# Kernel optimization log

Hardware: AMD Instinct MI355X
Metric: run time of the kernel (lower is better)

## Reference

```python
import jax, jax.numpy as jnp
import numpy as np

N_NODES = 50000
NODE_DIM = 128
HIDDEN = 128
N_EDGES = 1600000
N_POSTS = 8192


def setup_inputs() -> dict:
    key = jax.random.key(0)
    ks = jax.random.split(key, 12)
    glorot = lambda k, shp: jax.random.normal(k, shp, jnp.float32) * (1.0 / np.sqrt(shp[0]))
    inp = {
        "node_features": jax.random.normal(ks[0], (N_NODES, NODE_DIM), jnp.float32),
        "edge_index": jax.random.randint(ks[1], (2, N_EDGES), 0, N_NODES, jnp.int32),
        "post_mask": jax.random.randint(ks[2], (N_POSTS,), 0, N_NODES, jnp.int32),
        # node_encoder: node_dim -> hidden
        "W_enc": glorot(ks[3], (NODE_DIM, HIDDEN)),
        "b_enc": jnp.zeros((HIDDEN,), jnp.float32),
        # conv1/conv2: hidden -> hidden
        "W1": glorot(ks[4], (HIDDEN, HIDDEN)),
        "b1": jnp.zeros((HIDDEN,), jnp.float32),
        "W2": glorot(ks[5], (HIDDEN, HIDDEN)),
        "b2": jnp.zeros((HIDDEN,), jnp.float32),
        # output head: hidden -> hidden//2 -> 1
        "W_o1": glorot(ks[6], (HIDDEN, HIDDEN // 2)),
        "b_o1": jnp.zeros((HIDDEN // 2,), jnp.float32),
        "W_o2": glorot(ks[7], (HIDDEN // 2, 1)),
        "b_o2": jnp.zeros((1,), jnp.float32),
    }
    return inp


def _aggregate(h, src, dst, n_nodes):
    # sum_{e: dst[e]=v} h[src[e]]  -- vectorized scatter-add (segment_sum)
    return jax.ops.segment_sum(h[src], dst, num_segments=n_nodes)


def reference(node_features, edge_index, post_mask,
              W_enc, b_enc, W1, b1, W2, b2, W_o1, b_o1, W_o2, b_o2):
    src, dst = edge_index[0], edge_index[1]
    n = node_features.shape[0]

    h = jax.nn.relu(node_features @ W_enc + b_enc)          # [N, H]
    agg = _aggregate(h, src, dst, n)                        # [N, H]
    h = jax.nn.relu((agg + h) @ W1 + b1)
    agg = _aggregate(h, src, dst, n)
    h = jax.nn.relu((agg + h) @ W2 + b2)

    post = h[post_mask]                                     # [P, H]
    hid = jax.nn.relu(post @ W_o1 + b_o1)                   # [P, H//2]
    logits = (hid @ W_o2 + b_o2).squeeze(-1)                # [P]
    return jax.nn.sigmoid(logits)
```

## Files before the change

kernel.cpp:

```cpp
#include <hip/hip_runtime.h>
#include <math.h>


typedef unsigned long long u64;

#define RB_SIZE   4096
#define RB_ROUNDS 16

__global__ __launch_bounds__(256) void zero_kernel(int* __restrict__ p, int n) {
    int i = blockIdx.x * 256 + threadIdx.x;
    if (i < n) p[i] = 0;
}

__global__ __launch_bounds__(256) void hist_kernel(const int* __restrict__ dst,
                                                   int* __restrict__ counts, int E) {
    int e = blockIdx.x * 256 + threadIdx.x;
    if (e < E) atomicAdd(&counts[dst[e]], 1);
}

__global__ __launch_bounds__(1024) void scan_part(const int* __restrict__ in,
                                                  int* __restrict__ bsum, int n) {
    __shared__ int red[1024];
    int i = blockIdx.x * 1024 + threadIdx.x;
    red[threadIdx.x] = (i < n) ? in[i] : 0;
    __syncthreads();
    for (int d = 512; d; d >>= 1) {
        if (threadIdx.x < d) red[threadIdx.x] += red[threadIdx.x + d];
        __syncthreads();
    }
    if (threadIdx.x == 0) bsum[blockIdx.x] = red[0];
}

__global__ __launch_bounds__(256) void scan_tops_par(const int* __restrict__ bsum,
                                                     int* __restrict__ bbase, int nb,
                                                     int* __restrict__ total_out) {
    __shared__ int buf[256];
    int tid = threadIdx.x;
    int v = (tid < nb) ? bsum[tid] : 0;
    buf[tid] = v;
    __syncthreads();
    for (int s = 1; s < 256; s <<= 1) {
        int u = (tid >= s) ? buf[tid - s] : 0;
        __syncthreads();
        buf[tid] += u;
        __syncthreads();
    }
    if (tid < nb) bbase[tid] = buf[tid] - v;
    if (tid == 255 && total_out) *total_out = buf[255];
}

__global__ __launch_bounds__(1024) void scan_final(const int* __restrict__ in,
                                                   const int* __restrict__ bbase,
                                                   int* __restrict__ out, int n) {
    __shared__ int buf[1024];
    int tid = threadIdx.x;
    int i = blockIdx.x * 1024 + tid;
    int c = (i < n) ? in[i] : 0;
    buf[tid] = c;
    __syncthreads();
    for (int d = 1; d < 1024; d <<= 1) {
        int v = (tid >= d) ? buf[tid - d] : 0;
        __syncthreads();
        buf[tid] += v;
        __syncthreads();
    }
    if (i < n) out[i] = bbase[blockIdx.x] + buf[tid] - c;
}

template <bool FIRST>
__global__ __launch_bounds__(256) void radix_hist(const int* __restrict__ dstArr,
                                                  const u64* __restrict__ recIn,
                                                  int* __restrict__ blockhist,
                                                  int E, int NBLK) {
    __shared__ int cnt[256];
    cnt[threadIdx.x] = 0;
    __syncthreads();
    int base = blockIdx.x * RB_SIZE;
    for (int t = threadIdx.x; t < RB_SIZE; t += 256) {
        int i = base + t;
        if (i < E) {
            int d = FIRST ? (dstArr[i] & 255)
                          : (int)((recIn[i] >> 8) & 255);
            atomicAdd(&cnt[d], 1);
        }
    }
    __syncthreads();
    blockhist[threadIdx.x * NBLK + blockIdx.x] = cnt[threadIdx.x];
}

template <bool FIRST>
__global__ __launch_bounds__(256) void radix_scatter(const int* __restrict__ dstArr,
                                                     const int* __restrict__ srcArr,
                                                     const u64* __restrict__ recIn,
                                                     u64* __restrict__ recOut,
                                                     int* __restrict__ csr_src,
                                                     const int* __restrict__ blockbase,
                                                     int E, int NBLK) {
    __shared__ int cursor[256];
    __shared__ int gbase[256];
    __shared__ int cnt[256 * 4];
    __shared__ int wbase[256 * 4];
    int tid = threadIdx.x;
    int wid = tid >> 6, lane = tid & 63;
    cursor[tid] = 0;
    gbase[tid] = blockbase[tid * NBLK + blockIdx.x];
    int base = blockIdx.x * RB_SIZE;
    __syncthreads();
    for (int r = 0; r < RB_ROUNDS; ++r) {
        int i = base + r * 256 + tid;
        bool valid = (i < E);
        int d = 0;
        u64 rec = 0;
        if (valid) {
            if (FIRST) {
                int dv = dstArr[i];
                rec = ((u64)(unsigned)srcArr[i] << 32) | (unsigned)dv;
                d = dv & 255;
            } else {
                rec = recIn[i];
                d = (int)((rec >> 8) & 255);
            }
        }
        ((int4*)cnt)[tid] = make_int4(0, 0, 0, 0);
        u64 mask = ~0ull;
#pragma unroll
        for (int b = 0; b < 8; ++b) {
            int bit = (d >> b) & 1;
            u64 bal = __ballot(bit);
            mask &= bit ? bal : ~bal;
        }
        mask &= __ballot(valid ? 1 : 0);
        int rank = __popcll(mask & (((u64)1 << lane) - 1));
        int wtot = __popcll(mask);
        __syncthreads();
        if (valid && rank == 0) cnt[d * 4 + wid] = wtot;
        __syncthreads();
        {
            int run = cursor[tid];
#pragma unroll
            for (int w = 0; w < 4; ++w) {
                wbase[tid * 4 + w] = run;
                run += cnt[tid * 4 + w];
            }
            cursor[tid] = run;
        }
        __syncthreads();
        if (valid) {
            int pos = gbase[d] + wbase[d * 4 + wid] + rank;
            if (FIRST) recOut[pos] = rec;
            else       csr_src[pos] = (int)(rec >> 32);
        }
        __syncthreads();
    }
}

template <bool FUSE>
__global__ __launch_bounds__(256) void gemm128(const float* __restrict__ A,
                                               const float* __restrict__ A2,
                                               const float* __restrict__ W,
                                               const float* __restrict__ bias,
                                               float* __restrict__ out, int M) {
    __shared__ float Ws[64 * 128];
    __shared__ float As[32 * 128];
    int tid = threadIdx.x;
    int row0 = blockIdx.x * 32;

    float4* As4 = (float4*)As;
#pragma unroll
    for (int i = 0; i < 4; ++i) {
        int idx = tid + 256 * i;
        int r = idx >> 5, c = idx & 31;
        int gr = row0 + r;
        float4 v = make_float4(0.f, 0.f, 0.f, 0.f);
        if (gr < M) {
            v = ((const float4*)A)[gr * 32 + c];
            if (FUSE) {
                float4 u = ((const float4*)A2)[gr * 32 + c];
                v.x += u.x; v.y += u.y; v.z += u.z; v.w += u.w;
            }
        }
        As4[idx] = v;
    }

    int tx = tid & 31, ty = tid >> 5;
    float acc[4][4];
#pragma unroll
    for (int r = 0; r < 4; ++r)
#pragma unroll
        for (int c = 0; c < 4; ++c) acc[r][c] = 0.f;

    const float4* W4 = (const float4*)W;
    float4* Ws4 = (float4*)Ws;

    for (int kh = 0; kh < 2; ++kh) {
        __syncthreads();
#pragma unroll
        for (int i = 0; i < 8; ++i)
            Ws4[tid + 256 * i] = W4[kh * 2048 + tid + 256 * i];
        __syncthreads();

#pragma unroll 2
        for (int k = 0; k < 64; k += 4) {
            float4 a[4], b[4];
#pragma unroll
            for (int r = 0; r < 4; ++r)
                a[r] = *(const float4*)&As[(ty * 4 + r) * 128 + kh * 64 + k];
#pragma unroll
            for (int kk = 0; kk < 4; ++kk)
                b[kk] = *(const float4*)&Ws[(k + kk) * 128 + tx * 4];
#pragma unroll
            for (int r = 0; r < 4; ++r) {
                acc[r][0] = fmaf(a[r].x, b[0].x, acc[r][0]);
                acc[r][1] = fmaf(a[r].x, b[0].y, acc[r][1]);
                acc[r][2] = fmaf(a[r].x, b[0].z, acc[r][2]);
                acc[r][3] = fmaf(a[r].x, b[0].w, acc[r][3]);
                acc[r][0] = fmaf(a[r].y, b[1].x, acc[r][0]);
                acc[r][1] = fmaf(a[r].y, b[1].y, acc[r][1]);
                acc[r][2] = fmaf(a[r].y, b[1].z, acc[r][2]);
                acc[r][3] = fmaf(a[r].y, b[1].w, acc[r][3]);
                acc[r][0] = fmaf(a[r].z, b[2].x, acc[r][0]);
                acc[r][1] = fmaf(a[r].z, b[2].y, acc[r][1]);
                acc[r][2] = fmaf(a[r].z, b[2].z, acc[r][2]);
                acc[r][3] = fmaf(a[r].z, b[2].w, acc[r][3]);
                acc[r][0] = fmaf(a[r].w, b[3].x, acc[r][0]);
                acc[r][1] = fmaf(a[r].w, b[3].y, acc[r][1]);
                acc[r][2] = fmaf(a[r].w, b[3].z, acc[r][2]);
                acc[r][3] = fmaf(a[r].w, b[3].w, acc[r][3]);
            }
        }
    }

    float4 bv = *(const float4*)&bias[tx * 4];
#pragma unroll
    for (int r = 0; r < 4; ++r) {
        int gr = row0 + ty * 4 + r;
        if (gr < M) {
            float4 o;
            o.x = fmaxf(acc[r][0] + bv.x, 0.f);
            o.y = fmaxf(acc[r][1] + bv.y, 0.f);
            o.z = fmaxf(acc[r][2] + bv.z, 0.f);
            o.w = fmaxf(acc[r][3] + bv.w, 0.f);
            ((float4*)out)[gr * 32 + tx] = o;
        }
    }
}

__global__ __launch_bounds__(256) void aggregate_kernel(const float* __restrict__ h,
                                                        const int* __restrict__ offs,
                                                        const int* __restrict__ csr_src,
                                                        float* __restrict__ agg, int n) {
    int w = (blockIdx.x * 256 + threadIdx.x) >> 6;
    int lane = threadIdx.x & 63;
    int half = lane >> 5;
    int l32 = lane & 31;
    int node = w * 2 + half;
    bool nvalid = node < n;
    int beg = 0, deg = 0;
    if (nvalid) {
        beg = offs[node];
        deg = offs[node + 1] - beg;
    }
    int mdeg = max(deg, __shfl_xor(deg, 32));
    const float4* h4 = (const float4*)h;
    float ax = 0.f, ay = 0.f, az = 0.f, aw = 0.f;
    for (int base = 0; base < mdeg; base += 32) {
        int idx = base + l32;
        int sv = (nvalid && idx < deg) ? csr_src[beg + idx] : 0;
        int nk = mdeg - base; if (nk > 32) nk = 32;
#pragma unroll 4
        for (int j = 0; j < nk; ++j) {
            int s = __shfl(sv, (half << 5) | j);
            if (base + j < deg) {
                float4 r = h4[s * 32 + l32];
                ax += r.x; ay += r.y; az += r.z; aw += r.w;
            }
        }
    }
    if (nvalid) {
        float4 o = make_float4(ax, ay, az, aw);
        ((float4*)agg)[(size_t)node * 32 + l32] = o;
    }
}

__global__ __launch_bounds__(256) void head_kernel(const float* __restrict__ h,
                                                   const int* __restrict__ mask,
                                                   const float* __restrict__ Wo1,
                                                   const float* __restrict__ bo1,
                                                   const float* __restrict__ Wo2,
                                                   const float* __restrict__ bo2,
                                                   float* __restrict__ out, int P) {
    __shared__ float hids[4][64];
    int wid = threadIdx.x >> 6;
    int lane = threadIdx.x & 63;
    int p = blockIdx.x * 4 + wid;
    if (p >= P) return;
    int node = mask[p];
    const float* row = h + (size_t)node * 128;
    float acc = 0.f;
#pragma unroll 4
    for (int k = 0; k < 128; ++k)
        acc = fmaf(row[k], Wo1[k * 64 + lane], acc);
    hids[wid][lane] = fmaxf(acc + bo1[lane], 0.f);
    if (lane == 0) {
        double lg = 0.0;
        for (int j = 0; j < 64; ++j)
            lg = fma((double)hids[wid][j], (double)Wo2[j], lg);
        lg += (double)bo2[0];
        out[p] = (float)(1.0 / (1.0 + exp(-lg)));
    }
}

extern "C" void kernel_launch(void* const* d_in, const int* in_sizes, int n_in,
                              void* d_out, int out_size, void* d_ws, size_t ws_size,
                              hipStream_t stream) {
    const float* NF   = (const float*)d_in[0];
    const int*   EI   = (const int*)d_in[1];
    const int*   MASK = (const int*)d_in[2];
    const float* Wenc = (const float*)d_in[3];
    const float* benc = (const float*)d_in[4];
    const float* W1   = (const float*)d_in[5];
    const float* b1   = (const float*)d_in[6];
    const float* W2   = (const float*)d_in[7];
    const float* b2   = (const float*)d_in[8];
    const float* Wo1  = (const float*)d_in[9];
    const float* bo1  = (const float*)d_in[10];
    const float* Wo2  = (const float*)d_in[11];
    const float* bo2  = (const float*)d_in[12];
    float* out = (float*)d_out;

    const int N = in_sizes[0] / 128;
    const int E = in_sizes[1] / 2;
    const int P = in_sizes[2];

    char* ws = (char*)d_ws;
    size_t off = 0;
    auto alloc = [&](size_t bytes) {
        char* pp = ws + off;
        off += (bytes + 255) & ~(size_t)255;
        return pp;
    };
    float* h       = (float*)alloc((size_t)N * 128 * 4);
    float* agg     = (float*)alloc((size_t)N * 128 * 4);
    int*   offs    = (int*)alloc((size_t)(N + 1) * 4);
    int*   counts  = (int*)alloc((size_t)N * 4);
    int*   csr_src = (int*)alloc((size_t)E * 4);
    const int NBLK = (E + RB_SIZE - 1) / RB_SIZE;
    int*   bh      = (int*)alloc((size_t)256 * NBLK * 4);
    int*   bb      = (int*)alloc((size_t)256 * NBLK * 4);
    int*   bsum    = (int*)alloc(256 * 4);
    int*   bbase   = (int*)alloc(256 * 4);
    u64* rec_a = (u64*)h;
    u64* rec_b = (u64*)agg;

    const int* src = EI;
    const int* dst = EI + E;

    const int nscan = (N + 1023) / 1024;
    zero_kernel<<<(N + 255) / 256, 256, 0, stream>>>(counts, N);
    hist_kernel<<<(E + 255) / 256, 256, 0, stream>>>(dst, counts, E);
    scan_part<<<nscan, 1024, 0, stream>>>(counts, bsum, N);
    scan_tops_par<<<1, 256, 0, stream>>>(bsum, bbase, nscan, &offs[N]);
    scan_final<<<nscan, 1024, 0, stream>>>(counts, bbase, offs, N);

    const int L = 256 * NBLK;
    const int nscanL = (L + 1023) / 1024;
    radix_hist<true><<<NBLK, 256, 0, stream>>>(dst, nullptr, bh, E, NBLK);
    scan_part<<<nscanL, 1024, 0, stream>>>(bh, bsum, L);
    scan_tops_par<<<1, 256, 0, stream>>>(bsum, bbase, nscanL, nullptr);
    scan_final<<<nscanL, 1024, 0, stream>>>(bh, bbase, bb, L);
    radix_scatter<true><<<NBLK, 256, 0, stream>>>(dst, src, nullptr, rec_a, nullptr, bb, E, NBLK);
    radix_hist<false><<<NBLK, 256, 0, stream>>>(nullptr, rec_a, bh, E, NBLK);
    scan_part<<<nscanL, 1024, 0, stream>>>(bh, bsum, L);
    scan_tops_par<<<1, 256, 0, stream>>>(bsum, bbase, nscanL, nullptr);
    scan_final<<<nscanL, 1024, 0, stream>>>(bh, bbase, bb, L);
    radix_scatter<false><<<NBLK, 256, 0, stream>>>(nullptr, nullptr, rec_a, rec_b, csr_src, bb, E, NBLK);

    int gblocks = (N + 31) / 32;
    int ablocks = ((N + 1) / 2 + 3) / 4;
    gemm128<false><<<gblocks, 256, 0, stream>>>(NF, nullptr, Wenc, benc, h, N);
    aggregate_kernel<<<ablocks, 256, 0, stream>>>(h, offs, csr_src, agg, N);
    gemm128<true><<<gblocks, 256, 0, stream>>>(h, agg, W1, b1, h, N);
    aggregate_kernel<<<ablocks, 256, 0, stream>>>(h, offs, csr_src, agg, N);
    gemm128<true><<<gblocks, 256, 0, stream>>>(h, agg, W2, b2, h, N);
    head_kernel<<<(P + 3) / 4, 256, 0, stream>>>(h, MASK, Wo1, bo1, Wo2, bo2, out, P);
}
```

Measured before the change: 482.7 us.

## Split aggregation across column groups so each block gathers a 16-feature slice

The CSR aggregation kernel now splits the 128 features into 8 column groups of 16, with blockIdx selecting the column group and a 16-node tile. Each 16-lane group handles one node and gathers scalar floats per neighbor instead of float4 rows, and neighbor indices are broadcast with shuffles. The intent is that consecutive blocks touch one column slice of h, which may improve cache locality, and that the work spreads over more blocks. In exchange it uses 64-byte gathers instead of 512-byte rows, reads csr_src and offs 8 times over, and adds more shuffle and index overhead.

```diff
diff --git a/kernel.cpp b/kernel.cpp
--- a/kernel.cpp
+++ b/kernel.cpp
@@ -249,37 +249,37 @@
                                                         const int* __restrict__ offs,
                                                         const int* __restrict__ csr_src,
                                                         float* __restrict__ agg, int n) {
-    int w = (blockIdx.x * 256 + threadIdx.x) >> 6;
-    int lane = threadIdx.x & 63;
-    int half = lane >> 5;
-    int l32 = lane & 31;
-    int node = w * 2 + half;
+    int colg = blockIdx.x & 7;
+    int nb = blockIdx.x >> 3;
+    int tid = threadIdx.x;
+    int wid = tid >> 6;
+    int lane = tid & 63;
+    int g = (lane >> 4) & 3;
+    int l16 = lane & 15;
+    int node = nb * 16 + wid * 4 + g;
+    int f = colg * 16 + l16;
     bool nvalid = node < n;
     int beg = 0, deg = 0;
     if (nvalid) {
         beg = offs[node];
         deg = offs[node + 1] - beg;
     }
-    int mdeg = max(deg, __shfl_xor(deg, 32));
-    const float4* h4 = (const float4*)h;
-    float ax = 0.f, ay = 0.f, az = 0.f, aw = 0.f;
-    for (int base = 0; base < mdeg; base += 32) {
-        int idx = base + l32;
-        int sv = (nvalid && idx < deg) ? csr_src[beg + idx] : 0;
-        int nk = mdeg - base; if (nk > 32) nk = 32;
-#pragma unroll 4
-        for (int j = 0; j < nk; ++j) {
-            int s = __shfl(sv, (half << 5) | j);
-            if (base + j < deg) {
-                float4 r = h4[s * 32 + l32];
-                ax += r.x; ay += r.y; az += r.z; aw += r.w;
-            }
-        }
-    }
-    if (nvalid) {
-        float4 o = make_float4(ax, ay, az, aw);
-        ((float4*)agg)[(size_t)node * 32 + l32] = o;
-    }
+    int mdeg = deg;
+    mdeg = max(mdeg, __shfl_xor(mdeg, 16));
+    mdeg = max(mdeg, __shfl_xor(mdeg, 32));
+    float acc = 0.f;
+    for (int base = 0; base < mdeg; base += 16) {
+        int idx = base + l16;
+        int sv = (idx < deg) ? csr_src[beg + idx] : 0;
+        int nk = deg - base;
+#pragma unroll
+        for (int j = 0; j < 16; ++j) {
+            int s = __shfl(sv, (g << 4) | j);
+            if (j < nk)
+                acc += h[(size_t)((unsigned)s * 128 + f)];
+        }
+    }
+    if (nvalid) agg[(size_t)((unsigned)node * 128 + f)] = acc;
 }
 
 __global__ __launch_bounds__(256) void head_kernel(const float* __restrict__ h,
@@ -376,7 +376,7 @@
     radix_scatter<false><<<NBLK, 256, 0, stream>>>(nullptr, nullptr, rec_a, rec_b, csr_src, bb, E, NBLK);
 
     int gblocks = (N + 31) / 32;
-    int ablocks = ((N + 1) / 2 + 3) / 4;
+    int ablocks = ((N + 15) / 16) * 8;
     gemm128<false><<<gblocks, 256, 0, stream>>>(NF, nullptr, Wenc, benc, h, N);
     aggregate_kernel<<<ablocks, 256, 0, stream>>>(h, offs, csr_src, agg, N);
     gemm128<true><<<gblocks, 256, 0, stream>>>(h, agg, W1, b1, h, N);
```

Measured after the change: 672.3 us. 1.39x slower.
